# Performance work log

Measured on AMD Instinct MI355X. Metric: run time of the kernel, lower is better.

The kernel has to match this reference:

```python
import jax, jax.numpy as jnp
from jax import lax
import numpy as np

D_MODEL = 512
D_INNER = 1024      # expand=2
D_STATE = 256       # min(512, 256)
D_CONV = 4
DT_RANK = 32        # ceil(512/16)
N_FUSED = 64
EPS = 1e-5


def setup_inputs() -> dict:
    key = jax.random.key(0)
    ks = jax.random.split(key, 14)
    B, Lx = 4, 2048
    s = lambda k, shape: (jax.random.normal(k, shape, jnp.float32) * 0.02)
    return {
        "x": jax.random.normal(ks[0], (B, Lx, D_MODEL), jnp.float32),
        "fused_tokens": jax.random.normal(ks[1], (1, N_FUSED, D_MODEL), jnp.float32),
        "g1": jnp.ones((D_MODEL,), jnp.float32),
        "b1": jnp.zeros((D_MODEL,), jnp.float32),
        "g2": jnp.ones((D_MODEL,), jnp.float32),
        "b2": jnp.zeros((D_MODEL,), jnp.float32),
        "W_head": s(ks[2], (D_MODEL, D_MODEL)),
        "b_head": jnp.zeros((D_MODEL,), jnp.float32),
        "W_in": s(ks[3], (2 * D_INNER, D_MODEL)),          # in_proj, bias=False
        "W_conv": s(ks[4], (D_INNER, D_CONV)),             # depthwise causal conv
        "b_conv": s(ks[5], (D_INNER,)),
        "W_xp": s(ks[6], (DT_RANK + 2 * D_STATE, D_INNER)),  # x_proj, bias=False
        "W_dt": s(ks[7], (D_INNER, DT_RANK)),
        "b_dt": s(ks[8], (D_INNER,)),
        "A_log": jnp.log(jnp.broadcast_to(
            jnp.arange(1, D_STATE + 1, dtype=jnp.float32), (D_INNER, D_STATE))),
        "Dp": jnp.ones((D_INNER,), jnp.float32),           # skip parameter D
        "W_out": s(ks[9], (D_MODEL, D_INNER)),             # out_proj, bias=False
    }


def _ln(t, g, b):
    m = t.mean(-1, keepdims=True)
    v = t.var(-1, keepdims=True)
    return (t - m) * lax.rsqrt(v + EPS) * g + b


def _causal_dwconv(x, w, b):
    # x: (B, L, D); w: (D, K) depthwise kernel
    K = w.shape[1]
    xp = jnp.pad(x, ((0, 0), (K - 1, 0), (0, 0)))
    y = lax.conv_general_dilated(
        xp.transpose(0, 2, 1), w[:, None, :], (1,), 'VALID',
        feature_group_count=w.shape[0],
        dimension_numbers=('NCH', 'OIH', 'NCH'))
    return y.transpose(0, 2, 1) + b


def _selective_scan(u, delta, A, Bm, Cm, Dp):
    # u, delta: (B, L, Din); Bm, Cm: (B, L, N); A: (Din, N)
    B_, L, Din = u.shape
    N = A.shape[1]

    def step(h, inp):
        u_t, d_t, B_t, C_t = inp            # (B,Din),(B,Din),(B,N),(B,N)
        dA = jnp.exp(d_t[..., None] * A)    # (B, Din, N)
        h = dA * h + (d_t * u_t)[..., None] * B_t[:, None, :]
        y = jnp.einsum('bdn,bn->bd', h, C_t)
        return h, y

    h0 = jnp.zeros((B_, Din, N), u.dtype)
    xs = (u.transpose(1, 0, 2), delta.transpose(1, 0, 2),
          Bm.transpose(1, 0, 2), Cm.transpose(1, 0, 2))
    _, ys = lax.scan(step, h0, xs)
    return ys.transpose(1, 0, 2) + u * Dp


def reference(x, fused_tokens, g1, b1, g2, b2, W_head, b_head, W_in,
              W_conv, b_conv, W_xp, W_dt, b_dt, A_log, Dp, W_out):
    B = x.shape[0]
    toks = jnp.broadcast_to(fused_tokens, (B,) + fused_tokens.shape[1:])
    h = jnp.concatenate([x, toks], axis=1)          # (B, L, d)

    # --- Mamba block with pre-LN residual ---
    a = _ln(h, g1, b1)
    xz = a @ W_in.T                                 # (B, L, 2*Din)
    u, z = jnp.split(xz, 2, axis=-1)
    u = jax.nn.silu(_causal_dwconv(u, W_conv, b_conv))
    dbl = u @ W_xp.T                                # (B, L, dt_rank + 2N)
    dt, Bm, Cm = jnp.split(dbl, [DT_RANK, DT_RANK + D_STATE], axis=-1)
    delta = jax.nn.softplus(dt @ W_dt.T + b_dt)     # (B, L, Din)
    A = -jnp.exp(A_log)
    y = _selective_scan(u, delta, A, Bm, Cm, Dp)
    y = y * jax.nn.silu(z)
    h = y @ W_out.T + h

    # --- head with pre-LN residual ---
    h = _ln(h, g2, b2) @ W_head.T + b_head + h

    return h[:, -N_FUSED:, :]
```

## Files before the change

kernel.cpp:

```cpp
#include <hip/hip_runtime.h>

#define LTOT 2112
#define NROWS 8448
#define DM 512
#define DIN 1024
#define NST 256

using short8 = short  __attribute__((ext_vector_type(8)));
using f32x4  = float  __attribute__((ext_vector_type(4)));

__device__ __forceinline__ float fast_silu(float x){ return x / (1.f + __expf(-x)); }

__device__ __forceinline__ unsigned short f2bf(float f){
  unsigned u = __float_as_uint(f);
  unsigned r = (u + 0x7FFFu + ((u >> 16) & 1u)) >> 16;
  return (unsigned short)r;
}

__global__ __launch_bounds__(256) void ln1_kernel(
    const float* __restrict__ x, const float* __restrict__ toks,
    const float* __restrict__ g1, const float* __restrict__ b1,
    float* __restrict__ a, unsigned short* __restrict__ abf,
    unsigned short* __restrict__ a_last)
{
  int r = blockIdx.x;
  int bb = r / LTOT, t = r - bb*LTOT;
  const float* row = (t < 2048) ? (x + ((size_t)bb*2048 + t)*DM)
                                : (toks + (size_t)(t - 2048)*DM);
  int tid = threadIdx.x;
  float v0 = row[tid], v1 = row[tid + 256];
  float s = v0 + v1, sq = v0*v0 + v1*v1;
  #pragma unroll
  for (int o = 32; o > 0; o >>= 1){ s += __shfl_down(s,o); sq += __shfl_down(sq,o); }
  __shared__ float sb[8];
  if ((tid & 63) == 0){ sb[tid>>6] = s; sb[4 + (tid>>6)] = sq; }
  __syncthreads();
  float S  = sb[0]+sb[1]+sb[2]+sb[3];
  float SQ = sb[4]+sb[5]+sb[6]+sb[7];
  float mean = S * (1.f/DM);
  float var  = SQ * (1.f/DM) - mean*mean;
  float rs = rsqrtf(var + 1e-5f);
  size_t o0 = (size_t)r*DM;
  float r0 = (v0 - mean)*rs*g1[tid]       + b1[tid];
  float r1 = (v1 - mean)*rs*g1[tid + 256] + b1[tid + 256];
  a[o0 + tid]       = r0;
  a[o0 + tid + 256] = r1;
  unsigned short h0 = f2bf(r0), h1 = f2bf(r1);
  abf[o0 + tid]       = h0;
  abf[o0 + tid + 256] = h1;
  if (t >= 2048) {
    size_t lr = (size_t)(bb*64 + (t - 2048))*DM;
    a_last[lr + tid]       = h0;
    a_last[lr + tid + 256] = h1;
  }
}

__global__ __launch_bounds__(256) void f32_to_bf16_kernel(
    const float* __restrict__ in, unsigned short* __restrict__ out, int n4)
{
  int i = blockIdx.x*256 + threadIdx.x;
  if (i >= n4) return;
  float4 v = reinterpret_cast<const float4*>(in)[i];
  ushort4 o;
  o.x = f2bf(v.x); o.y = f2bf(v.y); o.z = f2bf(v.z); o.w = f2bf(v.w);
  reinterpret_cast<ushort4*>(out)[i] = o;
}

__global__ __launch_bounds__(256) void gemm_bf16(
    const unsigned short* __restrict__ A, const unsigned short* __restrict__ W,
    float* __restrict__ C, int M, int N, int K, int ldc)
{
  __shared__ unsigned short As[128][40];
  __shared__ unsigned short Bs[64][40];
  int tid  = threadIdx.x;
  int lane = tid & 63, wid = tid >> 6;
  int wm = wid >> 1, wn = wid & 1;
  int l15 = lane & 15, l4 = lane >> 4;
  int m0 = blockIdx.x * 128, n0 = blockIdx.y * 64;
  int sr = tid >> 2, sc = (tid & 3) * 8;

  f32x4 acc[4][2];
  #pragma unroll
  for (int i = 0; i < 4; ++i)
    #pragma unroll
    for (int j = 0; j < 2; ++j) acc[i][j] = (f32x4)0.f;

  for (int k0 = 0; k0 < K; k0 += 32) {
    #pragma unroll
    for (int rr = 0; rr < 2; ++rr) {
      int r = sr + rr*64;
      uint4 v = *reinterpret_cast<const uint4*>(A + (size_t)(m0 + r)*K + k0 + sc);
      *reinterpret_cast<uint4*>(&As[r][sc]) = v;
    }
    {
      int col = n0 + sr;
      uint4 v = make_uint4(0u,0u,0u,0u);
      if (col < N) v = *reinterpret_cast<const uint4*>(W + (size_t)col*K + k0 + sc);
      *reinterpret_cast<uint4*>(&Bs[sr][sc]) = v;
    }
    __syncthreads();
    short8 bfrag[2];
    #pragma unroll
    for (int fn = 0; fn < 2; ++fn)
      bfrag[fn] = *reinterpret_cast<const short8*>(&Bs[wn*32 + fn*16 + l15][l4*8]);
    #pragma unroll
    for (int fm = 0; fm < 4; ++fm) {
      short8 afrag = *reinterpret_cast<const short8*>(&As[wm*64 + fm*16 + l15][l4*8]);
      acc[fm][0] = __builtin_amdgcn_mfma_f32_16x16x32_bf16(afrag, bfrag[0], acc[fm][0], 0, 0, 0);
      acc[fm][1] = __builtin_amdgcn_mfma_f32_16x16x32_bf16(afrag, bfrag[1], acc[fm][1], 0, 0, 0);
    }
    __syncthreads();
  }
  #pragma unroll
  for (int fm = 0; fm < 4; ++fm)
    #pragma unroll
    for (int fn = 0; fn < 2; ++fn) {
      int col = n0 + wn*32 + fn*16 + l15;
      if (col < N)
        #pragma unroll
        for (int j = 0; j < 4; ++j) {
          int row = m0 + wm*64 + fm*16 + l4*4 + j;
          C[(size_t)row*ldc + col] = acc[fm][fn][j];
        }
    }
}

__global__ __launch_bounds__(256) void conv_silu_kernel(
    const float* __restrict__ upre, const float* __restrict__ Wc,
    const float* __restrict__ bc, float* __restrict__ u,
    unsigned short* __restrict__ ubf, unsigned short* __restrict__ u_last)
{
  size_t idx = (size_t)blockIdx.x*256 + threadIdx.x;
  int d = (int)(idx & 1023);
  int r = (int)(idx >> 10);
  int t = r % LTOT;
  float4 w4 = *reinterpret_cast<const float4*>(Wc + (size_t)d*4);
  float acc = bc[d];
  const float* up = upre + idx;
  if (t >= 3) acc = fmaf(up[-3*DIN], w4.x, acc);
  if (t >= 2) acc = fmaf(up[-2*DIN], w4.y, acc);
  if (t >= 1) acc = fmaf(up[-1*DIN], w4.z, acc);
  acc = fmaf(up[0], w4.w, acc);
  float res = fast_silu(acc);
  u[idx] = res;
  unsigned short hb = f2bf(res);
  ubf[idx] = hb;
  if (t >= 2048) {
    int bb = r / LTOT;
    u_last[(size_t)(bb*64 + (t - 2048))*DIN + d] = hb;
  }
}

__global__ __launch_bounds__(256) void delta_kernel(
    const float* __restrict__ dbl, const float* __restrict__ W_dt,
    const float* __restrict__ b_dt, const float* __restrict__ u,
    float* __restrict__ deltaT, float* __restrict__ duT)
{
  __shared__ float dts[32][33];
  __shared__ float wds[32][33];
  __shared__ float dT[32][33];
  __shared__ float uT[32][33];
  int r0 = blockIdx.x * 32;
  int d0 = blockIdx.y * 32;
  int bb = r0 / LTOT, t0 = r0 % LTOT;
  int tid = threadIdx.x;
  #pragma unroll
  for (int p = 0; p < 4; ++p) {
    int o = tid + p*256;
    int rl = o >> 5, j = o & 31;
    dts[rl][j] = dbl[(size_t)(r0 + rl)*288 + j];
    wds[rl][j] = W_dt[(size_t)(d0 + rl)*32 + j];
  }
  __syncthreads();
  #pragma unroll
  for (int p = 0; p < 4; ++p) {
    int o = tid + p*256;
    int dl = o & 31, rl = o >> 5;
    float acc = b_dt[d0 + dl];
    #pragma unroll
    for (int j = 0; j < 32; ++j) acc = fmaf(dts[rl][j], wds[dl][j], acc);
    float delta = (acc > 20.f) ? acc : __logf(1.f + __expf(acc));
    float uu = u[(size_t)(r0 + rl)*DIN + d0 + dl];
    dT[dl][rl] = delta;
    uT[dl][rl] = delta * uu;
  }
  __syncthreads();
  #pragma unroll
  for (int p = 0; p < 4; ++p) {
    int o = tid + p*256;
    int dl = o >> 5, ti = o & 31;
    size_t gi = ((size_t)bb*DIN + d0 + dl)*LTOT + t0 + ti;
    deltaT[gi] = dT[dl][ti];
    duT[gi]    = uT[dl][ti];
  }
}

__global__ __launch_bounds__(256) void scan_kernel(
    const float* __restrict__ deltaT, const float* __restrict__ duT,
    const float* __restrict__ dbl, const float* __restrict__ Cm,
    const float* __restrict__ A_log, float* __restrict__ y)
{
  int blk = blockIdx.x;
  int bb = blk >> 9;
  int d0 = (blk & 511) << 1;
  int n = threadIdx.x;
  float Ak[2], h[2] = {0.f, 0.f};
  #pragma unroll
  for (int g = 0; g < 2; ++g) {
    float al = A_log[(size_t)(d0+g)*NST + n];
    Ak[g] = -__builtin_amdgcn_exp2f(al * 1.44269504089f) * 1.44269504089f;
  }
  const size_t basebd = ((size_t)bb*DIN + d0)*LTOT;
  const float* __restrict__ pd = deltaT + basebd;
  const float* __restrict__ pu = duT    + basebd;
  const float* __restrict__ Bp = dbl + (size_t)bb*LTOT*288 + 32 + n;

  for (int t0c = 0; t0c < 2048; t0c += 4) {
    float Bnv[4];
    #pragma unroll
    for (int i = 0; i < 4; ++i) Bnv[i] = Bp[(size_t)(t0c + i)*288];
    float dv[2][4], uv[2][4];
    #pragma unroll
    for (int g = 0; g < 2; ++g) {
      float4 dq = *reinterpret_cast<const float4*>(pd + (size_t)g*LTOT + t0c);
      float4 uq = *reinterpret_cast<const float4*>(pu + (size_t)g*LTOT + t0c);
      dv[g][0]=dq.x; dv[g][1]=dq.y; dv[g][2]=dq.z; dv[g][3]=dq.w;
      uv[g][0]=uq.x; uv[g][1]=uq.y; uv[g][2]=uq.z; uv[g][3]=uq.w;
    }
    #pragma unroll
    for (int i = 0; i < 4; ++i) {
      float Bn = Bnv[i];
      #pragma unroll
      for (int g = 0; g < 2; ++g) {
        float dA = __builtin_amdgcn_exp2f(dv[g][i] * Ak[g]);
        h[g] = fmaf(dA, h[g], uv[g][i] * Bn);
      }
    }
  }

  __shared__ float red[4][2];
  for (int t = 2048; t < 2112; ++t) {
    float Bn = Bp[(size_t)t*288];
    #pragma unroll
    for (int g = 0; g < 2; ++g) {
      float dA = __builtin_amdgcn_exp2f(pd[(size_t)g*LTOT + t] * Ak[g]);
      h[g] = fmaf(dA, h[g], pu[(size_t)g*LTOT + t] * Bn);
    }
    float Cn = Cm[((size_t)(bb*64 + (t - 2048)))*NST + n];
    #pragma unroll
    for (int g = 0; g < 2; ++g) {
      float v = h[g] * Cn;
      #pragma unroll
      for (int o = 32; o > 0; o >>= 1) v += __shfl_down(v, o);
      if ((threadIdx.x & 63) == 0) red[threadIdx.x >> 6][g] = v;
    }
    __syncthreads();
    if (threadIdx.x < 2) {
      float sv = red[0][threadIdx.x] + red[1][threadIdx.x]
               + red[2][threadIdx.x] + red[3][threadIdx.x];
      y[((size_t)(bb*64 + (t - 2048)))*DIN + d0 + threadIdx.x] = sv;
    }
    __syncthreads();
  }
}

__global__ __launch_bounds__(256) void y2_kernel(
    const float* __restrict__ y, const float* __restrict__ u, const float* __restrict__ zs,
    const float* __restrict__ Dp, float* __restrict__ y2)
{
  int idx = blockIdx.x*256 + threadIdx.x;
  int rr = idx >> 10, d = idx & 1023;
  int bb = rr >> 6, tt = rr & 63;
  size_t r = (size_t)bb*LTOT + 2048 + tt;
  float yv = y[idx] + u[r*DIN + d] * Dp[d];
  y2[idx] = yv * fast_silu(zs[idx]);
}

__global__ __launch_bounds__(256) void outproj_kernel(
    const float* __restrict__ y2, const float* __restrict__ Wout,
    const float* __restrict__ toks, float* __restrict__ hfin)
{
  __shared__ float ys[4][DIN];
  int rb = blockIdx.x;
  int tid = threadIdx.x;
  #pragma unroll
  for (int rr = 0; rr < 4; ++rr)
    #pragma unroll
    for (int j = 0; j < 4; ++j)
      ys[rr][tid + j*256] = y2[(size_t)(rb*4 + rr)*DIN + tid + j*256];
  __syncthreads();
  #pragma unroll
  for (int cj = 0; cj < 2; ++cj) {
    int cidx = tid + cj*256;
    const float* wr = Wout + (size_t)cidx*DIN;
    float a0=0.f,a1=0.f,a2=0.f,a3=0.f;
    for (int k = 0; k < DIN; k += 4) {
      float4 w4 = *reinterpret_cast<const float4*>(wr + k);
      float4 r0 = *reinterpret_cast<const float4*>(&ys[0][k]);
      float4 r1 = *reinterpret_cast<const float4*>(&ys[1][k]);
      float4 r2 = *reinterpret_cast<const float4*>(&ys[2][k]);
      float4 r3 = *reinterpret_cast<const float4*>(&ys[3][k]);
      a0=fmaf(r0.x,w4.x,a0); a0=fmaf(r0.y,w4.y,a0); a0=fmaf(r0.z,w4.z,a0); a0=fmaf(r0.w,w4.w,a0);
      a1=fmaf(r1.x,w4.x,a1); a1=fmaf(r1.y,w4.y,a1); a1=fmaf(r1.z,w4.z,a1); a1=fmaf(r1.w,w4.w,a1);
      a2=fmaf(r2.x,w4.x,a2); a2=fmaf(r2.y,w4.y,a2); a2=fmaf(r2.z,w4.z,a2); a2=fmaf(r2.w,w4.w,a2);
      a3=fmaf(r3.x,w4.x,a3); a3=fmaf(r3.y,w4.y,a3); a3=fmaf(r3.z,w4.z,a3); a3=fmaf(r3.w,w4.w,a3);
    }
    float accs[4] = {a0,a1,a2,a3};
    #pragma unroll
    for (int rr = 0; rr < 4; ++rr) {
      int rg = rb*4 + rr;
      hfin[(size_t)rg*DM + cidx] = accs[rr] + toks[(size_t)(rg & 63)*DM + cidx];
    }
  }
}

__global__ __launch_bounds__(256) void head_kernel(
    const float* __restrict__ hfin, const float* __restrict__ g2, const float* __restrict__ b2,
    const float* __restrict__ Wh, const float* __restrict__ bh, float* __restrict__ out)
{
  int rr = blockIdx.x;
  int tid = threadIdx.x;
  float v0 = hfin[(size_t)rr*DM + tid];
  float v1 = hfin[(size_t)rr*DM + tid + 256];
  float s = v0 + v1, sq = v0*v0 + v1*v1;
  #pragma unroll
  for (int o = 32; o > 0; o >>= 1){ s += __shfl_down(s,o); sq += __shfl_down(sq,o); }
  __shared__ float sb[8];
  if ((tid & 63) == 0){ sb[tid>>6] = s; sb[4 + (tid>>6)] = sq; }
  __syncthreads();
  float S  = sb[0]+sb[1]+sb[2]+sb[3];
  float SQ = sb[4]+sb[5]+sb[6]+sb[7];
  float mean = S * (1.f/DM);
  float rs = rsqrtf(SQ * (1.f/DM) - mean*mean + 1e-5f);
  __shared__ float as[DM];
  as[tid]       = (v0 - mean)*rs*g2[tid]       + b2[tid];
  as[tid + 256] = (v1 - mean)*rs*g2[tid + 256] + b2[tid + 256];
  __syncthreads();
  #pragma unroll
  for (int cj = 0; cj < 2; ++cj) {
    int cidx = tid + cj*256;
    const float* wr = Wh + (size_t)cidx*DM;
    float acc = bh[cidx] + (cj ? v1 : v0);
    for (int k = 0; k < DM; k += 4) {
      float4 w4 = *reinterpret_cast<const float4*>(wr + k);
      float4 a4 = *reinterpret_cast<const float4*>(&as[k]);
      acc = fmaf(a4.x,w4.x,acc); acc = fmaf(a4.y,w4.y,acc);
      acc = fmaf(a4.z,w4.z,acc); acc = fmaf(a4.w,w4.w,acc);
    }
    out[(size_t)rr*DM + cidx] = acc;
  }
}

extern "C" void kernel_launch(void* const* d_in, const int* in_sizes, int n_in,
                              void* d_out, int out_size, void* d_ws, size_t ws_size,
                              hipStream_t stream) {
  const float* x      = (const float*)d_in[0];
  const float* toks   = (const float*)d_in[1];
  const float* g1     = (const float*)d_in[2];
  const float* b1     = (const float*)d_in[3];
  const float* g2     = (const float*)d_in[4];
  const float* b2     = (const float*)d_in[5];
  const float* W_head = (const float*)d_in[6];
  const float* b_head = (const float*)d_in[7];
  const float* W_in   = (const float*)d_in[8];
  const float* W_conv = (const float*)d_in[9];
  const float* b_conv = (const float*)d_in[10];
  const float* W_xp   = (const float*)d_in[11];
  const float* W_dt   = (const float*)d_in[12];
  const float* b_dt   = (const float*)d_in[13];
  const float* A_log  = (const float*)d_in[14];
  const float* Dp     = (const float*)d_in[15];
  const float* W_out  = (const float*)d_in[16];

  float* ws = (float*)d_ws;
  float* a_buf   = ws;
  float* u_pre   = a_buf   + (size_t)NROWS*DM;
  float* u_buf   = u_pre   + (size_t)NROWS*DIN;
  float* dbl_buf = u_buf   + (size_t)NROWS*DIN;
  float* duT     = dbl_buf + (size_t)NROWS*288;
  float* zs      = duT     + (size_t)NROWS*DIN;
  float* Cm      = zs      + (size_t)256*DIN;
  float* y_buf   = Cm      + (size_t)256*NST;
  float* y2_buf  = y_buf   + (size_t)256*DIN;
  float* hfin    = y2_buf  + (size_t)256*DIN;
  float* tail    = hfin    + (size_t)256*DM;
  float* deltaT  = u_pre;

  unsigned short* a_last_bf16 = (unsigned short*)tail;
  unsigned short* u_last_bf16 = a_last_bf16 + (size_t)256*DM;

  unsigned short* a_bf16  = (unsigned short*)duT;
  unsigned short* u_bf16  = a_bf16 + (size_t)NROWS*DM;
  unsigned short* wi_bf16 = u_bf16 + (size_t)NROWS*DIN;
  unsigned short* wx_bf16 = wi_bf16 + (size_t)2*DIN*DM;

  f32_to_bf16_kernel<<<(2*DIN*DM/4 + 255)/256, 256, 0, stream>>>(W_in, wi_bf16, 2*DIN*DM/4);
  f32_to_bf16_kernel<<<(544*DIN/4 + 255)/256, 256, 0, stream>>>(W_xp, wx_bf16, 544*DIN/4);

  ln1_kernel<<<NROWS, 256, 0, stream>>>(x, toks, g1, b1, a_buf, a_bf16, a_last_bf16);
  gemm_bf16<<<dim3(NROWS/128, DIN/64), 256, 0, stream>>>(a_bf16, wi_bf16, u_pre,
                                                         NROWS, DIN, DM, DIN);
  gemm_bf16<<<dim3(2, DIN/64), 256, 0, stream>>>(a_last_bf16, wi_bf16 + (size_t)DIN*DM,
                                                 zs, 256, DIN, DM, DIN);
  conv_silu_kernel<<<(NROWS*DIN)/256, 256, 0, stream>>>(u_pre, W_conv, b_conv,
                                                        u_buf, u_bf16, u_last_bf16);
  gemm_bf16<<<dim3(NROWS/128, (288 + 63)/64), 256, 0, stream>>>(u_bf16, wx_bf16, dbl_buf,
                                                                NROWS, 288, DIN, 288);
  gemm_bf16<<<dim3(2, NST/64), 256, 0, stream>>>(u_last_bf16, wx_bf16 + (size_t)288*DIN,
                                                 Cm, 256, NST, DIN, NST);
  delta_kernel<<<dim3(NROWS/32, DIN/32), 256, 0, stream>>>(dbl_buf, W_dt, b_dt, u_buf,
                                                           deltaT, duT);
  scan_kernel<<<2048, 256, 0, stream>>>(deltaT, duT, dbl_buf, Cm, A_log, y_buf);
  y2_kernel<<<1024, 256, 0, stream>>>(y_buf, u_buf, zs, Dp, y2_buf);
  outproj_kernel<<<64, 256, 0, stream>>>(y2_buf, W_out, toks, hfin);
  head_kernel<<<256, 256, 0, stream>>>(hfin, g2, b2, W_head, b_head, (float*)d_out);
}
```

Measured before the change: 709.1 us.

## Split scan to one channel per block, fuse y2 into outproj, drop fp32 LN store

The selective scan now assigns a single inner channel per 256-thread block and launches twice as many blocks, which shortens each block's serial work and raises parallelism for the latency-bound recurrence. The y2 gating (D skip plus silu(z)) is folded into the out-projection's shared-memory load, which removes a separate kernel launch and an intermediate buffer. The LayerNorm kernel no longer writes an unused fp32 copy of its output. As a trade-off, each block loads B values and runs the tail reduction for only one channel, so per-channel B traffic and syncthreads overhead double.

```diff
diff --git a/kernel.cpp b/kernel.cpp
--- a/kernel.cpp
+++ b/kernel.cpp
@@ -20,8 +20,7 @@
 __global__ __launch_bounds__(256) void ln1_kernel(
     const float* __restrict__ x, const float* __restrict__ toks,
     const float* __restrict__ g1, const float* __restrict__ b1,
-    float* __restrict__ a, unsigned short* __restrict__ abf,
-    unsigned short* __restrict__ a_last)
+    unsigned short* __restrict__ abf, unsigned short* __restrict__ a_last)
 {
   int r = blockIdx.x;
   int bb = r / LTOT, t = r - bb*LTOT;
@@ -43,8 +42,6 @@
   size_t o0 = (size_t)r*DM;
   float r0 = (v0 - mean)*rs*g1[tid]       + b1[tid];
   float r1 = (v1 - mean)*rs*g1[tid + 256] + b1[tid + 256];
-  a[o0 + tid]       = r0;
-  a[o0 + tid + 256] = r1;
   unsigned short h0 = f2bf(r0), h1 = f2bf(r1);
   abf[o0 + tid]       = h0;
   abf[o0 + tid + 256] = h1;
@@ -201,15 +198,12 @@
     const float* __restrict__ A_log, float* __restrict__ y)
 {
   int blk = blockIdx.x;
-  int bb = blk >> 9;
-  int d0 = (blk & 511) << 1;
+  int bb = blk >> 10;
+  int d0 = blk & 1023;
   int n = threadIdx.x;
-  float Ak[2], h[2] = {0.f, 0.f};
-  #pragma unroll
-  for (int g = 0; g < 2; ++g) {
-    float al = A_log[(size_t)(d0+g)*NST + n];
-    Ak[g] = -__builtin_amdgcn_exp2f(al * 1.44269504089f) * 1.44269504089f;
-  }
+  float al = A_log[(size_t)d0*NST + n];
+  float Ak = -__builtin_amdgcn_exp2f(al * 1.44269504089f) * 1.44269504089f;
+  float h = 0.f;
   const size_t basebd = ((size_t)bb*DIN + d0)*LTOT;
   const float* __restrict__ pd = deltaT + basebd;
   const float* __restrict__ pu = duT    + basebd;
@@ -219,75 +213,55 @@
     float Bnv[4];
     #pragma unroll
     for (int i = 0; i < 4; ++i) Bnv[i] = Bp[(size_t)(t0c + i)*288];
-    float dv[2][4], uv[2][4];
-    #pragma unroll
-    for (int g = 0; g < 2; ++g) {
-      float4 dq = *reinterpret_cast<const float4*>(pd + (size_t)g*LTOT + t0c);
-      float4 uq = *reinterpret_cast<const float4*>(pu + (size_t)g*LTOT + t0c);
-      dv[g][0]=dq.x; dv[g][1]=dq.y; dv[g][2]=dq.z; dv[g][3]=dq.w;
-      uv[g][0]=uq.x; uv[g][1]=uq.y; uv[g][2]=uq.z; uv[g][3]=uq.w;
-    }
+    float4 dq = *reinterpret_cast<const float4*>(pd + t0c);
+    float4 uq = *reinterpret_cast<const float4*>(pu + t0c);
+    float dv[4] = {dq.x, dq.y, dq.z, dq.w};
+    float uv[4] = {uq.x, uq.y, uq.z, uq.w};
     #pragma unroll
     for (int i = 0; i < 4; ++i) {
-      float Bn = Bnv[i];
-      #pragma unroll
-      for (int g = 0; g < 2; ++g) {
-        float dA = __builtin_amdgcn_exp2f(dv[g][i] * Ak[g]);
-        h[g] = fmaf(dA, h[g], uv[g][i] * Bn);
-      }
-    }
-  }
-
-  __shared__ float red[4][2];
+      float dA = __builtin_amdgcn_exp2f(dv[i] * Ak);
+      h = fmaf(dA, h, uv[i] * Bnv[i]);
+    }
+  }
+
+  __shared__ float red[4];
   for (int t = 2048; t < 2112; ++t) {
-    float Bn = Bp[(size_t)t*288];
-    #pragma unroll
-    for (int g = 0; g < 2; ++g) {
-      float dA = __builtin_amdgcn_exp2f(pd[(size_t)g*LTOT + t] * Ak[g]);
-      h[g] = fmaf(dA, h[g], pu[(size_t)g*LTOT + t] * Bn);
-    }
+    float dA = __builtin_amdgcn_exp2f(pd[t] * Ak);
+    h = fmaf(dA, h, pu[t] * Bp[(size_t)t*288]);
     float Cn = Cm[((size_t)(bb*64 + (t - 2048)))*NST + n];
-    #pragma unroll
-    for (int g = 0; g < 2; ++g) {
-      float v = h[g] * Cn;
-      #pragma unroll
-      for (int o = 32; o > 0; o >>= 1) v += __shfl_down(v, o);
-      if ((threadIdx.x & 63) == 0) red[threadIdx.x >> 6][g] = v;
-    }
+    float v = h * Cn;
+    #pragma unroll
+    for (int o = 32; o > 0; o >>= 1) v += __shfl_down(v, o);
+    if ((threadIdx.x & 63) == 0) red[threadIdx.x >> 6] = v;
     __syncthreads();
-    if (threadIdx.x < 2) {
-      float sv = red[0][threadIdx.x] + red[1][threadIdx.x]
-               + red[2][threadIdx.x] + red[3][threadIdx.x];
-      y[((size_t)(bb*64 + (t - 2048)))*DIN + d0 + threadIdx.x] = sv;
-    }
+    if (threadIdx.x == 0)
+      y[((size_t)(bb*64 + (t - 2048)))*DIN + d0] = red[0] + red[1] + red[2] + red[3];
     __syncthreads();
   }
 }
 
-__global__ __launch_bounds__(256) void y2_kernel(
-    const float* __restrict__ y, const float* __restrict__ u, const float* __restrict__ zs,
-    const float* __restrict__ Dp, float* __restrict__ y2)
-{
-  int idx = blockIdx.x*256 + threadIdx.x;
-  int rr = idx >> 10, d = idx & 1023;
-  int bb = rr >> 6, tt = rr & 63;
-  size_t r = (size_t)bb*LTOT + 2048 + tt;
-  float yv = y[idx] + u[r*DIN + d] * Dp[d];
-  y2[idx] = yv * fast_silu(zs[idx]);
-}
-
 __global__ __launch_bounds__(256) void outproj_kernel(
-    const float* __restrict__ y2, const float* __restrict__ Wout,
-    const float* __restrict__ toks, float* __restrict__ hfin)
+    const float* __restrict__ y, const float* __restrict__ u,
+    const float* __restrict__ zs, const float* __restrict__ Dp,
+    const float* __restrict__ Wout, const float* __restrict__ toks,
+    float* __restrict__ hfin)
 {
   __shared__ float ys[4][DIN];
   int rb = blockIdx.x;
   int tid = threadIdx.x;
   #pragma unroll
-  for (int rr = 0; rr < 4; ++rr)
-    #pragma unroll
-    for (int j = 0; j < 4; ++j)
-      ys[rr][tid + j*256] = y2[(size_t)(rb*4 + rr)*DIN + tid + j*256];
+  for (int rr = 0; rr < 4; ++rr) {
+    int rg = rb*4 + rr;
+    int bbb = rg >> 6, tt = rg & 63;
+    size_t rfull = (size_t)bbb*LTOT + 2048 + tt;
+    #pragma unroll
+    for (int j = 0; j < 4; ++j) {
+      int d = tid + j*256;
+      size_t idx = (size_t)rg*DIN + d;
+      float yv = y[idx] + u[rfull*DIN + d] * Dp[d];
+      ys[rr][d] = yv * fast_silu(zs[idx]);
+    }
+  }
   __syncthreads();
   #pragma unroll
   for (int cj = 0; cj < 2; ++cj) {
@@ -397,7 +371,7 @@
   f32_to_bf16_kernel<<<(2*DIN*DM/4 + 255)/256, 256, 0, stream>>>(W_in, wi_bf16, 2*DIN*DM/4);
   f32_to_bf16_kernel<<<(544*DIN/4 + 255)/256, 256, 0, stream>>>(W_xp, wx_bf16, 544*DIN/4);
 
-  ln1_kernel<<<NROWS, 256, 0, stream>>>(x, toks, g1, b1, a_buf, a_bf16, a_last_bf16);
+  ln1_kernel<<<NROWS, 256, 0, stream>>>(x, toks, g1, b1, a_bf16, a_last_bf16);
   gemm_bf16<<<dim3(NROWS/128, DIN/64), 256, 0, stream>>>(a_bf16, wi_bf16, u_pre,
                                                          NROWS, DIN, DM, DIN);
   gemm_bf16<<<dim3(2, DIN/64), 256, 0, stream>>>(a_last_bf16, wi_bf16 + (size_t)DIN*DM,
@@ -410,8 +384,7 @@
                                                  Cm, 256, NST, DIN, NST);
   delta_kernel<<<dim3(NROWS/32, DIN/32), 256, 0, stream>>>(dbl_buf, W_dt, b_dt, u_buf,
                                                            deltaT, duT);
-  scan_kernel<<<2048, 256, 0, stream>>>(deltaT, duT, dbl_buf, Cm, A_log, y_buf);
-  y2_kernel<<<1024, 256, 0, stream>>>(y_buf, u_buf, zs, Dp, y2_buf);
-  outproj_kernel<<<64, 256, 0, stream>>>(y2_buf, W_out, toks, hfin);
+  scan_kernel<<<4096, 256, 0, stream>>>(deltaT, duT, dbl_buf, Cm, A_log, y_buf);
+  outproj_kernel<<<64, 256, 0, stream>>>(y_buf, u_buf, zs, Dp, W_out, toks, hfin);
   head_kernel<<<256, 256, 0, stream>>>(hfin, g2, b2, W_head, b_head, (float*)d_out);
 }
```

Measured after the change: 756.0 us. +6.6%, slower.
